# Performance work log

Measured on AMD Instinct MI355X. Metric: run time of the kernel, lower is better.

## Reference

```python
import jax, jax.numpy as jnp
import numpy as np
import math

N_HEADS = 4
IN_DIM = 1024
DIM_HEAD = IN_DIM // N_HEADS


def setup_inputs() -> dict:
    key = jax.random.key(0)
    ks = jax.random.split(key, 5)
    x = jax.random.normal(ks[0], (8, 2048, IN_DIM), dtype=jnp.float32)
    std = 0.02
    W_Q = jax.random.normal(ks[1], (N_HEADS, IN_DIM, DIM_HEAD), dtype=jnp.float32) * std
    W_K = jax.random.normal(ks[2], (N_HEADS, IN_DIM, DIM_HEAD), dtype=jnp.float32) * std
    W_V = jax.random.normal(ks[3], (N_HEADS, IN_DIM, DIM_HEAD), dtype=jnp.float32) * std
    W_O = jax.random.normal(ks[4], (N_HEADS, DIM_HEAD, IN_DIM), dtype=jnp.float32) * std
    b_Q = jnp.zeros((N_HEADS, DIM_HEAD), dtype=jnp.float32)
    b_K = jnp.zeros((N_HEADS, DIM_HEAD), dtype=jnp.float32)
    b_V = jnp.zeros((N_HEADS, DIM_HEAD), dtype=jnp.float32)
    b_O = jnp.zeros((IN_DIM,), dtype=jnp.float32)
    return {"normalized_resid_pre": x, "W_Q": W_Q, "b_Q": b_Q, "W_K": W_K,
            "b_K": b_K, "W_V": W_V, "b_V": b_V, "W_O": W_O, "b_O": b_O}


def reference(normalized_resid_pre, W_Q, b_Q, W_K, b_K, W_V, b_V, W_O, b_O):
    x = normalized_resid_pre  # [n, s, d_model]
    # projections: [n, s, h, dh]
    q = jnp.einsum('nsd,hde->nshe', x, W_Q) + b_Q
    k = jnp.einsum('nsd,hde->nshe', x, W_K) + b_K
    v = jnp.einsum('nsd,hde->nshe', x, W_V) + b_V
    scale = 1.0 / math.sqrt(DIM_HEAD)
    scores = jnp.einsum('nqhe,nkhe->nhqk', q, k) * scale  # [n, h, q, k]
    pattern = jax.nn.softmax(scores, axis=-1)
    z = jnp.einsum('nhqk,nkhe->nqhe', pattern, v)  # [n, q, h, dh]
    out = jnp.einsum('nqhe,hed->nqd', z, W_O) + b_O  # [n, q, d_model]
    return out
```

## Files before the change

### kernel.cpp

```cpp
#include <hip/hip_runtime.h>

typedef __attribute__((ext_vector_type(8))) short short8;
typedef __attribute__((ext_vector_type(4))) float floatx4;
typedef __attribute__((ext_vector_type(16))) float floatx16;
typedef __attribute__((ext_vector_type(4))) unsigned short ushort4v;
typedef __attribute__((ext_vector_type(2))) unsigned int uint2v;
typedef unsigned short u16;

__device__ __forceinline__ u16 f2bf(float f) {
  unsigned u = __float_as_uint(f);
  u += 0x7fffu + ((u >> 16) & 1u);
  return (u16)(u >> 16);
}

__device__ __forceinline__ void gl_lds16(const void* g, void* l) {
  __builtin_amdgcn_global_load_lds((const __attribute__((address_space(1))) void*)g,
                                   (__attribute__((address_space(3))) void*)l, 16, 0, 0);
}

__device__ __forceinline__ float bpermf(float v, int srclane) {
  return __int_as_float(__builtin_amdgcn_ds_bpermute(srclane << 2, __float_as_int(v)));
}

#define BARRIER() do { asm volatile("" ::: "memory"); __builtin_amdgcn_s_barrier(); asm volatile("" ::: "memory"); } while (0)


__global__ void k_cvt_x(const float* __restrict__ x, u16* __restrict__ o, long n) {
  long i = ((long)blockIdx.x * blockDim.x + threadIdx.x) * 8;
  long stride = (long)gridDim.x * blockDim.x * 8;
  for (; i < n; i += stride) {
    float4 a = *(const float4*)(x + i);
    float4 b = *(const float4*)(x + i + 4);
    ushort4v r0 = { f2bf(a.x), f2bf(a.y), f2bf(a.z), f2bf(a.w) };
    ushort4v r1 = { f2bf(b.x), f2bf(b.y), f2bf(b.z), f2bf(b.w) };
    *(ushort4v*)(o + i) = r0;
    *(ushort4v*)(o + i + 4) = r1;
  }
}

__global__ __launch_bounds__(256) void k_cvt_w(
    const float* __restrict__ WQ, const float* __restrict__ WK,
    const float* __restrict__ WV, const float* __restrict__ WO,
    u16* __restrict__ wqkv, u16* __restrict__ wo) {
  __shared__ float tile[64][65];
  const int bid = blockIdx.x;
  const float* src;
  u16* dst;
  int C, R, r0, c0;
  if (bid < 768) {
    int th = bid >> 6;
    int tid6 = bid & 63;
    int t = th >> 2, h = th & 3;
    src = ((t == 0) ? WQ : (t == 1) ? WK : WV) + h * 1024 * 256;
    dst = wqkv + (size_t)(t * 1024 + h * 256) * 1024;
    R = 1024; C = 256;
    r0 = (tid6 & 15) * 64;
    c0 = (tid6 >> 4) * 64;
  } else {
    int tid6 = bid - 768;
    src = WO; dst = wo;
    R = 1024; C = 1024;
    r0 = (tid6 & 15) * 64;
    c0 = (tid6 >> 4) * 64;
  }
  const int tx = threadIdx.x & 15, ty = threadIdx.x >> 4;
#pragma unroll
  for (int i = 0; i < 4; ++i) {
    int r = ty + 16 * i;
    float4 v = *(const float4*)(src + (long)(r0 + r) * C + c0 + tx * 4);
    tile[r][tx * 4 + 0] = v.x;
    tile[r][tx * 4 + 1] = v.y;
    tile[r][tx * 4 + 2] = v.z;
    tile[r][tx * 4 + 3] = v.w;
  }
  __syncthreads();
#pragma unroll
  for (int i = 0; i < 4; ++i) {
    int c = ty + 16 * i;
    ushort4v o = { f2bf(tile[tx * 4 + 0][c]), f2bf(tile[tx * 4 + 1][c]),
                   f2bf(tile[tx * 4 + 2][c]), f2bf(tile[tx * 4 + 3][c]) };
    *(ushort4v*)(dst + (long)(c0 + c) * R + r0 + tx * 4) = o;
  }
}

template<int EPI>
__global__ __launch_bounds__(512, 2) void k_gemm8(
    const u16* __restrict__ A, const u16* __restrict__ Bt,
    u16* __restrict__ Qo, u16* __restrict__ Ko, u16* __restrict__ Vt,
    const float* __restrict__ bQ, const float* __restrict__ bK, const float* __restrict__ bV,
    float* __restrict__ out, const float* __restrict__ bO, int gridNx) {
  extern __shared__ char lds[];
  const int tid = threadIdx.x, lane = tid & 63, w = tid >> 6;
  const int wm = w >> 2, wn = w & 3;
  const int cI = lane & 15, rI = lane >> 4;
  const int bid = blockIdx.x;
  const int xcd = bid & 7, ii = bid >> 3;
  const int by = xcd * 8 + (ii & 7);
  const int bx = ii >> 3;
  (void)gridNx;
  const long am0 = (long)by * 256, bn0 = (long)bx * 256;

  int so_ds[2], so_src[2];
#pragma unroll
  for (int jj = 0; jj < 2; ++jj) {
    int o = jj * 8192 + tid * 16;
    int row = o >> 7;
    so_ds[jj] = o;
    so_src[jj] = row * 1024 + ((((o >> 4) & 7) ^ (row & 7)) << 3);
  }
  const u16* gAlo = A + am0 * 1024;
  const u16* gAhi = gAlo + 128 * 1024;
  const u16* gBlo = Bt + bn0 * 1024;
  const u16* gBhi = gBlo + 128 * 1024;

#define STG(gp, kt, ldsbyte) do { \
    gl_lds16((gp) + (kt) * 64 + so_src[0], lds + (ldsbyte) + so_ds[0]); \
    gl_lds16((gp) + (kt) * 64 + so_src[1], lds + (ldsbyte) + so_ds[1]); \
  } while (0)

  floatx4 acc[8][4] = {};

  STG(gAlo, 0, 0);
  STG(gBlo, 0, 65536);
  STG(gAhi, 0, 16384);
  STG(gBhi, 0, 81920);
  STG(gAlo, 1, 32768);
  STG(gBlo, 1, 98304);
  asm volatile("s_waitcnt vmcnt(4)" ::: "memory");
  BARRIER();

#define PHASE(AB, BB, MH, NH, STAGE_STMT, VMSTMT) do { \
    short8 af[4][2], bf[2][2]; \
    _Pragma("unroll") \
    for (int mi2 = 0; mi2 < 4; ++mi2) { \
      int row = wm * 64 + mi2 * 16 + cI; \
      const char* rp = lds + (AB) + (MH) * 16384 + row * 128; \
      int sw = row & 7; \
      _Pragma("unroll") \
      for (int kk = 0; kk < 2; ++kk) \
        af[mi2][kk] = *(const short8*)(rp + (((kk * 4 + rI) ^ sw) << 4)); \
    } \
    _Pragma("unroll") \
    for (int ni2 = 0; ni2 < 2; ++ni2) { \
      int row = wn * 32 + ni2 * 16 + cI; \
      const char* rp = lds + (BB) + (NH) * 16384 + row * 128; \
      int sw = row & 7; \
      _Pragma("unroll") \
      for (int kk = 0; kk < 2; ++kk) \
        bf[ni2][kk] = *(const short8*)(rp + (((kk * 4 + rI) ^ sw) << 4)); \
    } \
    STAGE_STMT; \
    VMSTMT; \
    BARRIER(); \
    __builtin_amdgcn_s_setprio(1); \
    _Pragma("unroll") \
    for (int mi2 = 0; mi2 < 4; ++mi2) \
      _Pragma("unroll") \
      for (int ni2 = 0; ni2 < 2; ++ni2) \
        _Pragma("unroll") \
        for (int kk = 0; kk < 2; ++kk) \
          acc[(MH) * 4 + mi2][(NH) * 2 + ni2] = __builtin_amdgcn_mfma_f32_16x16x32_bf16( \
              af[mi2][kk], bf[ni2][kk], acc[(MH) * 4 + mi2][(NH) * 2 + ni2], 0, 0, 0); \
    __builtin_amdgcn_s_setprio(0); \
    BARRIER(); \
  } while (0)

  for (int it = 0; it < 8; ++it) {
    const int u = 2 * it;
    const bool s2 = (u + 2 < 16), s3 = (u + 3 < 16);
    PHASE(0, 65536, 0, 0, STG(gAhi, u + 1, 49152), );
    PHASE(0, 65536, 0, 1, STG(gBhi, u + 1, 114688), );
    PHASE(0, 65536, 1, 0, if (s2) STG(gAlo, u + 2, 0), );
    PHASE(0, 65536, 1, 1, if (s2) STG(gBlo, u + 2, 65536),
          if (s2) { asm volatile("s_waitcnt vmcnt(4)" ::: "memory"); }
          else    { asm volatile("s_waitcnt vmcnt(0)" ::: "memory"); });
    PHASE(32768, 98304, 0, 0, if (s2) STG(gAhi, u + 2, 16384), );
    PHASE(32768, 98304, 0, 1, if (s2) STG(gBhi, u + 2, 81920), );
    PHASE(32768, 98304, 1, 0, if (s3) STG(gAlo, u + 3, 32768), );
    PHASE(32768, 98304, 1, 1, if (s3) STG(gBlo, u + 3, 98304),
          asm volatile("s_waitcnt vmcnt(4)" ::: "memory"));
  }

  if (EPI == 0) {
    const int t = (int)(bn0 >> 10);
    const int h = (int)(bn0 >> 8) & 3;
    const float* bias = (t == 0) ? bQ : (t == 1) ? bK : bV;
    const float sc = (t == 0) ? 0.0625f * 1.44269504088896f : 1.0f;
#pragma unroll
    for (int MH = 0; MH < 2; ++MH)
#pragma unroll
    for (int mi = 0; mi < 4; ++mi) {
      int m = (int)am0 + MH * 128 + wm * 64 + mi * 16 + rI * 4;
      int b = m >> 11, s = m & 2047;
#pragma unroll
      for (int NH = 0; NH < 2; ++NH)
#pragma unroll
      for (int ni = 0; ni < 2; ++ni) {
        int e = NH * 128 + wn * 32 + ni * 16 + cI;
        float bb = bias[h * 256 + e];
        floatx4 c = acc[MH * 4 + mi][NH * 2 + ni];
        if (t == 0) {
          long base = ((long)(b * 4 + h) * 2048 + s) * 256 + e;
          Qo[base]       = f2bf((c[0] + bb) * sc);
          Qo[base + 256] = f2bf((c[1] + bb) * sc);
          Qo[base + 512] = f2bf((c[2] + bb) * sc);
          Qo[base + 768] = f2bf((c[3] + bb) * sc);
        } else if (t == 1) {
          long kb = ((long)(b * 4 + h) << 19) + ((long)(s >> 5) << 13) +
                    ((e >> 3) << 8) + ((s & 31) << 3) + (e & 7);
          Ko[kb]      = f2bf(c[0] + bb);
          Ko[kb + 8]  = f2bf(c[1] + bb);
          Ko[kb + 16] = f2bf(c[2] + bb);
          Ko[kb + 24] = f2bf(c[3] + bb);
        } else {
          long vb = ((long)(b * 4 + h) << 19) + ((long)(s >> 5) << 13) +
                    (((s >> 3) & 3) << 11) + ((long)e << 3) + (s & 7);
          ushort4v v = { f2bf(c[0] + bb), f2bf(c[1] + bb), f2bf(c[2] + bb), f2bf(c[3] + bb) };
          *(ushort4v*)(Vt + vb) = v;
        }
      }
    }
  } else {
#pragma unroll
    for (int MH = 0; MH < 2; ++MH)
#pragma unroll
    for (int mi = 0; mi < 4; ++mi) {
      int m = (int)am0 + MH * 128 + wm * 64 + mi * 16 + rI * 4;
#pragma unroll
      for (int NH = 0; NH < 2; ++NH)
#pragma unroll
      for (int ni = 0; ni < 2; ++ni) {
        int n = (int)bn0 + NH * 128 + wn * 32 + ni * 16 + cI;
        float bb = bO[n];
        floatx4 c = acc[MH * 4 + mi][NH * 2 + ni];
        out[(long)m * 1024 + n]       = c[0] + bb;
        out[(long)(m + 1) * 1024 + n] = c[1] + bb;
        out[(long)(m + 2) * 1024 + n] = c[2] + bb;
        out[(long)(m + 3) * 1024 + n] = c[3] + bb;
      }
    }
  }
#undef PHASE
#undef STG
}

__global__ __launch_bounds__(512, 1) void k_attn(
    const u16* __restrict__ Q, const u16* __restrict__ K,
    const u16* __restrict__ Vt, u16* __restrict__ Z) {
  extern __shared__ u16 smem[];
  char* sKc = (char*)smem;
  char* sVc = (char*)smem + 32768;
  const int tid = threadIdx.x, lane = tid & 63, w = tid >> 6;
  const int q = lane & 31, hi = lane >> 5;
  const int xcd = blockIdx.x & 7, bi = blockIdx.x >> 3;
  const int bh = xcd * 4 + (bi & 3);
  const int qt = bi >> 2;
  const long base = (long)bh * 2048 * 256;
  const int q0 = qt * 256 + w * 32;

  const u16* Kg0 = K + base;
  const u16* Vg0 = Vt + base;
  const int stq = tid * 8;
  const int dtq = tid * 16;

  short8 qf[16];
#pragma unroll
  for (int ec = 0; ec < 16; ++ec)
    qf[ec] = *(const short8*)(Q + base + (long)(q0 + q) * 256 + ec * 16 + hi * 8);

#define STAGE_K(kt_, buf_) do { \
    const u16* g_ = Kg0 + (kt_) * 8192 + stq; \
    char* d_ = sKc + (buf_) * 16384 + dtq; \
    gl_lds16(g_, d_); \
    gl_lds16(g_ + 4096, d_ + 8192); \
  } while (0)
#define STAGE_V(kt_, buf_) do { \
    const u16* g_ = Vg0 + (kt_) * 8192 + stq; \
    char* d_ = sVc + (buf_) * 16384 + dtq; \
    gl_lds16(g_, d_); \
    gl_lds16(g_ + 4096, d_ + 8192); \
  } while (0)

  STAGE_K(0, 0);

  floatx16 z[8] = {};
  float m_run = -1e30f, l = 0.f;
  const int kb = hi * 512 + q * 16;
  const int vb = hi * 4096 + q * 16;
  short8 pa0 = {}, pa1 = {};

  __syncthreads();

  for (int t = 0; t < 64; ++t) {
    const int cb = t & 1;
    if (t < 63) STAGE_K(t + 1, cb ^ 1);
    STAGE_V(t, cb);
    const char* pK = sKc + cb * 16384 + kb;
    const char* pV = sVc + (cb ^ 1) * 16384 + vb;

    floatx16 s0 = {}, s1 = {};
    __builtin_amdgcn_s_setprio(1);
    if (t > 0) {
#pragma unroll
      for (int u = 0; u < 8; ++u) {
        short8 kf0 = *(const short8*)(pK + (2 * u) * 1024);
        s0 = __builtin_amdgcn_mfma_f32_32x32x16_bf16(kf0, qf[2 * u], s0, 0, 0, 0);
        short8 vf0 = *(const short8*)(pV + u * 512);
        z[u] = __builtin_amdgcn_mfma_f32_32x32x16_bf16(pa0, vf0, z[u], 0, 0, 0);
        short8 kf1 = *(const short8*)(pK + (2 * u + 1) * 1024);
        s1 = __builtin_amdgcn_mfma_f32_32x32x16_bf16(kf1, qf[2 * u + 1], s1, 0, 0, 0);
        short8 vf1 = *(const short8*)(pV + 8192 + u * 512);
        z[u] = __builtin_amdgcn_mfma_f32_32x32x16_bf16(pa1, vf1, z[u], 0, 0, 0);
      }
    } else {
#pragma unroll
      for (int u = 0; u < 8; ++u) {
        short8 kf0 = *(const short8*)(pK + (2 * u) * 1024);
        s0 = __builtin_amdgcn_mfma_f32_32x32x16_bf16(kf0, qf[2 * u], s0, 0, 0, 0);
        short8 kf1 = *(const short8*)(pK + (2 * u + 1) * 1024);
        s1 = __builtin_amdgcn_mfma_f32_32x32x16_bf16(kf1, qf[2 * u + 1], s1, 0, 0, 0);
      }
    }
    __builtin_amdgcn_s_setprio(0);
    floatx16 s = s0 + s1;

    float m0 = fmaxf(s[0], s[1]),  m1 = fmaxf(s[2], s[3]);
    float m2 = fmaxf(s[4], s[5]),  m3 = fmaxf(s[6], s[7]);
    float m4 = fmaxf(s[8], s[9]),  m5 = fmaxf(s[10], s[11]);
    float m6 = fmaxf(s[12], s[13]), m7 = fmaxf(s[14], s[15]);
    m0 = fmaxf(m0, m1); m2 = fmaxf(m2, m3); m4 = fmaxf(m4, m5); m6 = fmaxf(m6, m7);
    m0 = fmaxf(m0, m2); m4 = fmaxf(m4, m6);
    float pm = fmaxf(m0, m4);
    {
      uint2v sw = __builtin_amdgcn_permlane32_swap(__float_as_uint(pm), __float_as_uint(pm), false, false);
      pm = fmaxf(__uint_as_float(sw[0]), __uint_as_float(sw[1]));
    }

    if (!__all(pm <= m_run + 8.f)) {
      float mn = fmaxf(m_run, pm);
      float esc = exp2f(m_run - mn);
      l *= esc;
      m_run = mn;
      float escv[16];
#pragma unroll
      for (int r = 0; r < 16; ++r)
        escv[r] = bpermf(esc, ((r & 3) + 8 * (r >> 2) + 4 * hi) + 32 * hi);
#pragma unroll
      for (int et = 0; et < 8; ++et)
#pragma unroll
        for (int r = 0; r < 16; ++r) z[et][r] *= escv[r];
    }

    float p[16];
#pragma unroll
    for (int r = 0; r < 16; ++r) p[r] = exp2f(s[r] - m_run);
    float a0 = p[0] + p[1], a1 = p[2] + p[3], a2 = p[4] + p[5], a3 = p[6] + p[7];
    float a4 = p[8] + p[9], a5 = p[10] + p[11], a6 = p[12] + p[13], a7 = p[14] + p[15];
    a0 += a1; a2 += a3; a4 += a5; a6 += a7;
    a0 += a2; a4 += a6;
    float rs = a0 + a4;
    {
      uint2v sw = __builtin_amdgcn_permlane32_swap(__float_as_uint(rs), __float_as_uint(rs), false, false);
      l += __uint_as_float(sw[0]) + __uint_as_float(sw[1]);
    }

    unsigned w0, w1, w2, w3, w4, w5, w6, w7;
    asm("v_cvt_pk_bf16_f32 %0, %1, %2" : "=v"(w0) : "v"(p[0]), "v"(p[1]));
    asm("v_cvt_pk_bf16_f32 %0, %1, %2" : "=v"(w1) : "v"(p[2]), "v"(p[3]));
    asm("v_cvt_pk_bf16_f32 %0, %1, %2" : "=v"(w2) : "v"(p[4]), "v"(p[5]));
    asm("v_cvt_pk_bf16_f32 %0, %1, %2" : "=v"(w3) : "v"(p[6]), "v"(p[7]));
    asm("v_cvt_pk_bf16_f32 %0, %1, %2" : "=v"(w4) : "v"(p[8]), "v"(p[9]));
    asm("v_cvt_pk_bf16_f32 %0, %1, %2" : "=v"(w5) : "v"(p[10]), "v"(p[11]));
    asm("v_cvt_pk_bf16_f32 %0, %1, %2" : "=v"(w6) : "v"(p[12]), "v"(p[13]));
    asm("v_cvt_pk_bf16_f32 %0, %1, %2" : "=v"(w7) : "v"(p[14]), "v"(p[15]));
    uint2v e02 = __builtin_amdgcn_permlane32_swap(w0, w2, false, false);
    uint2v e13 = __builtin_amdgcn_permlane32_swap(w1, w3, false, false);
    uint2v e46 = __builtin_amdgcn_permlane32_swap(w4, w6, false, false);
    uint2v e57 = __builtin_amdgcn_permlane32_swap(w5, w7, false, false);
    int4 t0i = { (int)e02[0], (int)e13[0], (int)e02[1], (int)e13[1] };
    int4 t1i = { (int)e46[0], (int)e57[0], (int)e46[1], (int)e57[1] };
    pa0 = *(short8*)&t0i;
    pa1 = *(short8*)&t1i;

    __syncthreads();
  }

  {
    const char* pV = sVc + 16384 + vb;
#pragma unroll
    for (int u = 0; u < 8; ++u) {
      short8 vf0 = *(const short8*)(pV + u * 512);
      z[u] = __builtin_amdgcn_mfma_f32_32x32x16_bf16(pa0, vf0, z[u], 0, 0, 0);
      short8 vf1 = *(const short8*)(pV + 8192 + u * 512);
      z[u] = __builtin_amdgcn_mfma_f32_32x32x16_bf16(pa1, vf1, z[u], 0, 0, 0);
    }
  }

  float linv = 1.f / l;
  float invv[16];
#pragma unroll
  for (int r = 0; r < 16; ++r)
    invv[r] = bpermf(linv, ((r & 3) + 8 * (r >> 2) + 4 * hi) + 32 * hi);

  const int b = bh >> 2, hh = bh & 3;
  const long zb = (long)b * 2048 * 1024 + hh * 256;
#pragma unroll
  for (int r = 0; r < 16; ++r) {
    const int qr = (r & 3) + 8 * (r >> 2) + 4 * hi;
    long rb = zb + (long)(q0 + qr) * 1024;
#pragma unroll
    for (int et = 0; et < 8; ++et)
      Z[rb + et * 32 + q] = f2bf(z[et][r] * invv[r]);
  }
#undef STAGE_K
#undef STAGE_V
}


extern "C" void kernel_launch(void* const* d_in, const int* in_sizes, int n_in,
                              void* d_out, int out_size, void* d_ws, size_t ws_size,
                              hipStream_t stream) {
  const float* x  = (const float*)d_in[0];
  const float* WQ = (const float*)d_in[1];
  const float* bQ = (const float*)d_in[2];
  const float* WK = (const float*)d_in[3];
  const float* bK = (const float*)d_in[4];
  const float* WV = (const float*)d_in[5];
  const float* bV = (const float*)d_in[6];
  const float* WO = (const float*)d_in[7];
  const float* bO = (const float*)d_in[8];
  float* out = (float*)d_out;

  char* p = (char*)d_ws;
  u16* xb   = (u16*)p; p += (size_t)16384 * 1024 * 2;
  u16* wqkv = (u16*)p; p += (size_t)3072 * 1024 * 2;
  u16* wo   = (u16*)p; p += (size_t)1024 * 1024 * 2;
  u16* Qb   = (u16*)p; p += (size_t)32 * 2048 * 256 * 2;
  u16* Kb   = (u16*)p; p += (size_t)32 * 2048 * 256 * 2;
  u16* Vtb  = (u16*)p; p += (size_t)32 * 256 * 2048 * 2;
  u16* Zb   = xb;

  const int attn_lds = 65536;
  (void)hipFuncSetAttribute((const void*)k_attn,
                            hipFuncAttributeMaxDynamicSharedMemorySize, attn_lds);
  const int gemm_lds = 131072;
  (void)hipFuncSetAttribute((const void*)k_gemm8<0>,
                            hipFuncAttributeMaxDynamicSharedMemorySize, gemm_lds);
  (void)hipFuncSetAttribute((const void*)k_gemm8<1>,
                            hipFuncAttributeMaxDynamicSharedMemorySize, gemm_lds);

  k_cvt_x<<<dim3(4096), dim3(256), 0, stream>>>(x, xb, (long)16384 * 1024);
  k_cvt_w<<<dim3(1024), dim3(256), 0, stream>>>(WQ, WK, WV, WO, wqkv, wo);
  k_gemm8<0><<<dim3(768), dim3(512), gemm_lds, stream>>>(xb, wqkv, Qb, Kb, Vtb, bQ, bK, bV,
                                                         (float*)nullptr, (const float*)nullptr, 12);
  k_attn<<<dim3(256), dim3(512), attn_lds, stream>>>(Qb, Kb, Vtb, Zb);
  k_gemm8<1><<<dim3(256), dim3(512), gemm_lds, stream>>>(Zb, wo,
                                                         (u16*)nullptr, (u16*)nullptr, (u16*)nullptr,
                                                         (const float*)nullptr, (const float*)nullptr, (const float*)nullptr,
                                                         out, bO, 4);
}
```

Before: 324.6 us.

## Merge conversion kernels and split attention into smaller 4-wave blocks

The x and weight fp32-to-bf16 conversions now run in one launch instead of two, saving a kernel launch and its tail. The attention kernel changes from 512-thread blocks covering 256 queries to 256-thread blocks covering 128 queries, with a 512-block grid and two blocks allowed per CU. This gives finer scheduling and better load balance across XCDs, but each block now stages K/V itself, so K/V traffic and LDS staging per query double. The row-max reduction is also reshaped into 3-input max trees, which may map to v_max3.

```diff
diff --git a/kernel.cpp b/kernel.cpp
--- a/kernel.cpp
+++ b/kernel.cpp
@@ -24,32 +24,34 @@
 
 #define BARRIER() do { asm volatile("" ::: "memory"); __builtin_amdgcn_s_barrier(); asm volatile("" ::: "memory"); } while (0)
 
-
-__global__ void k_cvt_x(const float* __restrict__ x, u16* __restrict__ o, long n) {
-  long i = ((long)blockIdx.x * blockDim.x + threadIdx.x) * 8;
-  long stride = (long)gridDim.x * blockDim.x * 8;
-  for (; i < n; i += stride) {
-    float4 a = *(const float4*)(x + i);
-    float4 b = *(const float4*)(x + i + 4);
-    ushort4v r0 = { f2bf(a.x), f2bf(a.y), f2bf(a.z), f2bf(a.w) };
-    ushort4v r1 = { f2bf(b.x), f2bf(b.y), f2bf(b.z), f2bf(b.w) };
-    *(ushort4v*)(o + i) = r0;
-    *(ushort4v*)(o + i + 4) = r1;
-  }
-}
-
-__global__ __launch_bounds__(256) void k_cvt_w(
+__global__ __launch_bounds__(256) void k_cvt(
+    const float* __restrict__ x, u16* __restrict__ xb,
     const float* __restrict__ WQ, const float* __restrict__ WK,
     const float* __restrict__ WV, const float* __restrict__ WO,
     u16* __restrict__ wqkv, u16* __restrict__ wo) {
   __shared__ float tile[64][65];
   const int bid = blockIdx.x;
+  if (bid < 4096) {
+    const long n = (long)16384 * 1024;
+    long i = ((long)bid * blockDim.x + threadIdx.x) * 8;
+    long stride = (long)4096 * blockDim.x * 8;
+    for (; i < n; i += stride) {
+      float4 a = *(const float4*)(x + i);
+      float4 b = *(const float4*)(x + i + 4);
+      ushort4v r0 = { f2bf(a.x), f2bf(a.y), f2bf(a.z), f2bf(a.w) };
+      ushort4v r1 = { f2bf(b.x), f2bf(b.y), f2bf(b.z), f2bf(b.w) };
+      *(ushort4v*)(xb + i) = r0;
+      *(ushort4v*)(xb + i + 4) = r1;
+    }
+    return;
+  }
+  const int wb = bid - 4096;
   const float* src;
   u16* dst;
   int C, R, r0, c0;
-  if (bid < 768) {
-    int th = bid >> 6;
-    int tid6 = bid & 63;
+  if (wb < 768) {
+    int th = wb >> 6;
+    int tid6 = wb & 63;
     int t = th >> 2, h = th & 3;
     src = ((t == 0) ? WQ : (t == 1) ? WK : WV) + h * 1024 * 256;
     dst = wqkv + (size_t)(t * 1024 + h * 256) * 1024;
@@ -57,7 +59,7 @@
     r0 = (tid6 & 15) * 64;
     c0 = (tid6 >> 4) * 64;
   } else {
-    int tid6 = bid - 768;
+    int tid6 = wb - 768;
     src = WO; dst = wo;
     R = 1024; C = 1024;
     r0 = (tid6 & 15) * 64;
@@ -244,7 +246,7 @@
 #undef STG
 }
 
-__global__ __launch_bounds__(512, 1) void k_attn(
+__global__ __launch_bounds__(256, 2) void k_attn(
     const u16* __restrict__ Q, const u16* __restrict__ K,
     const u16* __restrict__ Vt, u16* __restrict__ Z) {
   extern __shared__ u16 smem[];
@@ -252,11 +254,10 @@
   char* sVc = (char*)smem + 32768;
   const int tid = threadIdx.x, lane = tid & 63, w = tid >> 6;
   const int q = lane & 31, hi = lane >> 5;
-  const int xcd = blockIdx.x & 7, bi = blockIdx.x >> 3;
-  const int bh = xcd * 4 + (bi & 3);
-  const int qt = bi >> 2;
+  const int role = (blockIdx.x & 7) * 64 + (blockIdx.x >> 3);
+  const int bh = role >> 4, qt = role & 15;
   const long base = (long)bh * 2048 * 256;
-  const int q0 = qt * 256 + w * 32;
+  const int q0 = qt * 128 + w * 32;
 
   const u16* Kg0 = K + base;
   const u16* Vg0 = Vt + base;
@@ -271,14 +272,14 @@
 #define STAGE_K(kt_, buf_) do { \
     const u16* g_ = Kg0 + (kt_) * 8192 + stq; \
     char* d_ = sKc + (buf_) * 16384 + dtq; \
-    gl_lds16(g_, d_); \
-    gl_lds16(g_ + 4096, d_ + 8192); \
+    _Pragma("unroll") \
+    for (int j = 0; j < 4; ++j) gl_lds16(g_ + j * 2048, d_ + j * 4096); \
   } while (0)
 #define STAGE_V(kt_, buf_) do { \
     const u16* g_ = Vg0 + (kt_) * 8192 + stq; \
     char* d_ = sVc + (buf_) * 16384 + dtq; \
-    gl_lds16(g_, d_); \
-    gl_lds16(g_ + 4096, d_ + 8192); \
+    _Pragma("unroll") \
+    for (int j = 0; j < 4; ++j) gl_lds16(g_ + j * 2048, d_ + j * 4096); \
   } while (0)
 
   STAGE_K(0, 0);
@@ -324,13 +325,12 @@
     __builtin_amdgcn_s_setprio(0);
     floatx16 s = s0 + s1;
 
-    float m0 = fmaxf(s[0], s[1]),  m1 = fmaxf(s[2], s[3]);
-    float m2 = fmaxf(s[4], s[5]),  m3 = fmaxf(s[6], s[7]);
-    float m4 = fmaxf(s[8], s[9]),  m5 = fmaxf(s[10], s[11]);
-    float m6 = fmaxf(s[12], s[13]), m7 = fmaxf(s[14], s[15]);
-    m0 = fmaxf(m0, m1); m2 = fmaxf(m2, m3); m4 = fmaxf(m4, m5); m6 = fmaxf(m6, m7);
-    m0 = fmaxf(m0, m2); m4 = fmaxf(m4, m6);
-    float pm = fmaxf(m0, m4);
+    float t0 = fmaxf(fmaxf(s[0], s[1]), s[2]);
+    float t1 = fmaxf(fmaxf(s[3], s[4]), s[5]);
+    float t2 = fmaxf(fmaxf(s[6], s[7]), s[8]);
+    float t3 = fmaxf(fmaxf(s[9], s[10]), s[11]);
+    float t4 = fmaxf(fmaxf(s[12], s[13]), s[14]);
+    float pm = fmaxf(fmaxf(t0, t1), fmaxf(fmaxf(t2, t3), fmaxf(t4, s[15])));
     {
       uint2v sw = __builtin_amdgcn_permlane32_swap(__float_as_uint(pm), __float_as_uint(pm), false, false);
       pm = fmaxf(__uint_as_float(sw[0]), __uint_as_float(sw[1]));
@@ -449,11 +449,10 @@
   (void)hipFuncSetAttribute((const void*)k_gemm8<1>,
                             hipFuncAttributeMaxDynamicSharedMemorySize, gemm_lds);
 
-  k_cvt_x<<<dim3(4096), dim3(256), 0, stream>>>(x, xb, (long)16384 * 1024);
-  k_cvt_w<<<dim3(1024), dim3(256), 0, stream>>>(WQ, WK, WV, WO, wqkv, wo);
+  k_cvt<<<dim3(5120), dim3(256), 0, stream>>>(x, xb, WQ, WK, WV, WO, wqkv, wo);
   k_gemm8<0><<<dim3(768), dim3(512), gemm_lds, stream>>>(xb, wqkv, Qb, Kb, Vtb, bQ, bK, bV,
                                                          (float*)nullptr, (const float*)nullptr, 12);
-  k_attn<<<dim3(256), dim3(512), attn_lds, stream>>>(Qb, Kb, Vtb, Zb);
+  k_attn<<<dim3(512), dim3(256), attn_lds, stream>>>(Qb, Kb, Vtb, Zb);
   k_gemm8<1><<<dim3(256), dim3(512), gemm_lds, stream>>>(Zb, wo,
                                                          (u16*)nullptr, (u16*)nullptr, (u16*)nullptr,
                                                          (const float*)nullptr, (const float*)nullptr, (const float*)nullptr,
```

New measurement: 324.2 us. Within noise of the previous version (-0.1%).
